# Optimization experiments

Measured on AMD Instinct MI355X. Metric: run time of the kernel, lower is better.

## Reference

```python
import jax, jax.numpy as jnp
import numpy as np

B, T, N, F_IN = 2, 4, 1024, 256
H, N_HIDDEN = 8, 128
SLOPE = 0.2
NEG_INF = -9e16


def setup_inputs() -> dict:
    key = jax.random.key(0)
    k1, k2, k3, k4 = jax.random.split(key, 4)
    h = jax.random.normal(k1, (B, T, N, F_IN), dtype=jnp.float32)
    adj_mat = jax.random.randint(k2, (N, N), 0, 2, dtype=jnp.int32)
    W = jax.random.normal(k3, (F_IN, H * N_HIDDEN), dtype=jnp.float32) * 0.05
    a = jax.random.normal(k4, (H, 2 * N_HIDDEN, 1), dtype=jnp.float32) * 0.05
    return {"h": h, "adj_mat": adj_mat, "W": W, "a": a}


def reference(h, adj_mat, W, a):
    b, t, n, _ = h.shape
    # linear transform: [B,T,N,F_in] @ [F_in, H*nh] -> [B,T,N,H*nh]
    ht = jnp.einsum('btjs,sh->btjh', h, W)
    # dropout is identity in eval mode
    ht = ht.reshape(b, t, n, H, N_HIDDEN).transpose(0, 1, 3, 2, 4)  # [B,T,H,N,nh]
    # additive attention scores
    a_src = a[:, :N_HIDDEN, :]   # [H, nh, 1]
    a_tgt = a[:, N_HIDDEN:, :]   # [H, nh, 1]
    src = jnp.einsum('bthnd,hdo->bthno', ht, a_src)  # [B,T,H,N,1]
    tgt = jnp.einsum('bthnd,hdo->bthno', ht, a_tgt)  # [B,T,H,N,1]
    e = src + jnp.swapaxes(tgt, -1, -2)              # [B,T,H,N,N]
    e = jnp.where(e >= 0, e, SLOPE * e)              # LeakyReLU
    e = jnp.where(adj_mat > 0, e, jnp.float32(NEG_INF))
    attention = jax.nn.softmax(e, axis=-1)
    # weighted aggregation: [B,T,H,N,N] @ [B,T,H,N,nh]
    h_prime = jnp.einsum('bthij,bthjd->bthid', attention, ht)
    # concat=False branch: mean over dim 0 (batch), as in the source
    return h_prime.mean(axis=0)  # [T,H,N,nh]
```

## Files before the change

### kernel.cpp

```cpp
#include <hip/hip_runtime.h>
#include <cstddef>
#include <cstdint>

#define B_ 2
#define T_ 4
#define N_ 1024
#define FIN_ 256
#define H_ 8
#define D_ 128
#define L2E_ 1.4426950408889634f

typedef __attribute__((ext_vector_type(8))) short short8;
typedef __attribute__((ext_vector_type(4))) float f32x4;

#define MFMA16(A, B, C) __builtin_amdgcn_mfma_f32_16x16x32_bf16((A), (B), (C), 0, 0, 0)

__device__ __forceinline__ unsigned short f2bf(float f) {
    uint32_t u = __float_as_uint(f);
    uint32_t r = (u + 0x7fffu + ((u >> 16) & 1u)) >> 16;
    return (unsigned short)r;
}

__device__ __forceinline__ uint32_t cvt_pk_bf16(float lo, float hi) {
    uint32_t r;
    asm volatile("v_cvt_pk_bf16_f32 %0, %1, %2" : "=v"(r) : "v"(lo), "v"(hi));
    return r;
}

__device__ __forceinline__ float fexp2(float x) {
#if __has_builtin(__builtin_amdgcn_exp2f)
    return __builtin_amdgcn_exp2f(x);
#else
    float r;
    asm("v_exp_f32 %0, %1" : "=v"(r) : "v"(x));
    return r;
#endif
}

__device__ __forceinline__ void load_lds16(const unsigned short* g, unsigned short* l) {
    __builtin_amdgcn_global_load_lds(
        (const __attribute__((address_space(1))) uint32_t*)g,
        (__attribute__((address_space(3))) uint32_t*)l, 16, 0, 0);
}

__global__ __launch_bounds__(256) void k_prep(const int* __restrict__ adj,
                                              const float* __restrict__ W,
                                              const float* __restrict__ a,
                                              unsigned short* __restrict__ Wt_bf,
                                              uint32_t* __restrict__ adjbits,
                                              float* __restrict__ wa) {
    __shared__ float wl[64][68];
    const int bid = blockIdx.x, tid = threadIdx.x;
    if (bid < 128) {
        const int w = bid * 256 + tid;
        const int i = w >> 5, jw = w & 31;
        const int4* p = (const int4*)(adj + (size_t)i * N_ + jw * 32);
        uint32_t bits = 0;
        #pragma unroll
        for (int q = 0; q < 8; ++q) {
            const int4 v = p[q];
            bits |= (uint32_t)(v.x > 0) << (q * 4 + 0);
            bits |= (uint32_t)(v.y > 0) << (q * 4 + 1);
            bits |= (uint32_t)(v.z > 0) << (q * 4 + 2);
            bits |= (uint32_t)(v.w > 0) << (q * 4 + 3);
        }
        adjbits[w] = bits;
    } else if (bid < 192) {
        const int tb  = bid - 128;
        const int hk0 = (tb >> 2) * 64;
        const int s0  = (tb & 3) * 64;
        {
            const int r  = tid >> 2;
            const int c0 = (tid & 3) * 16;
            #pragma unroll
            for (int k = 0; k < 4; ++k)
                *(float4*)&wl[r][c0 + k * 4] =
                    *(const float4*)(W + (size_t)(s0 + r) * (H_ * D_) + hk0 + c0 + k * 4);
        }
        __syncthreads();
        {
            const int r2 = tid >> 2;
            const int c2 = (tid & 3) * 16;
            unsigned short ob[16];
            #pragma unroll
            for (int k = 0; k < 16; ++k) ob[k] = f2bf(wl[c2 + k][r2]);
            unsigned short* dst = Wt_bf + (size_t)(hk0 + r2) * FIN_ + s0 + c2;
            *(uint4*)(dst)     = *(uint4*)&ob[0];
            *(uint4*)(dst + 8) = *(uint4*)&ob[8];
        }
    } else {
        const int o    = (bid - 192) * 256 + tid;
        const int head = o >> 9;
        const int st   = (o >> 8) & 1;
        const int s    = o & 255;
        const float* wr = W + (size_t)s * (H_ * D_) + head * D_;
        const float* ar = a + head * 256 + st * 128;
        float sum = 0.f;
        #pragma unroll
        for (int d = 0; d < 128; d += 4) {
            const float4 wv = *(const float4*)(wr + d);
            const float4 av = *(const float4*)(ar + d);
            sum += wv.x * av.x + wv.y * av.y + wv.z * av.z + wv.w * av.w;
        }
        wa[s * 16 + head * 2 + st] = sum;
    }
}

__global__ __launch_bounds__(256, 2) void k_gemm_sp(const float* __restrict__ h,
                                                    const unsigned short* __restrict__ Wt_bf,
                                                    const float* __restrict__ wa,
                                                    unsigned short* __restrict__ htT,
                                                    float* __restrict__ s1, float* __restrict__ s2,
                                                    float* __restrict__ t1, float* __restrict__ t2) {
    __shared__ __align__(16) char smem[24576];
    const int bid = blockIdx.x, tid = threadIdx.x;
    if (bid < 1024) {
        unsigned short* a_lds = (unsigned short*)smem;
        unsigned short* b_lds = (unsigned short*)(smem + 16384);
        const int xcd  = bid & 7;
        const int slot = bid >> 3;
        const int gid  = xcd * 8 + (slot >> 4);
        const int bt   = gid >> 3;
        const int n0   = (gid & 7) * 128;
        const int hk0  = (slot & 15) * 64;
        const int w = tid >> 6, lane = tid & 63;
        const int row16 = lane & 15, kgrp = lane >> 4;
        const int kswz = (kgrp ^ ((row16 >> 1) & 3)) * 8;
        const int ar  = tid >> 1;
        const int akh = tid & 1;
        const int asub = ar >> 4, arow = ar & 15;
        const int ax = (arow >> 1) & 3;
        const int aslot0 = ((akh * 2) ^ ax) * 8;
        const int aslot1 = ((akh * 2 + 1) ^ ax) * 8;
        const float* ga = h + ((size_t)bt * N_ + n0 + ar) * FIN_ + akh * 16;
        unsigned short* aw_ = a_lds + asub * 512 + arow * 32;
        const int brow = lane >> 2;
        const int bsb  = (lane & 3) ^ ((lane >> 3) & 3);
        const unsigned short* gb = Wt_bf + (size_t)(hk0 + w * 16 + brow) * FIN_ + bsb * 8;
        unsigned short* bw_ = b_lds + w * 512 + (size_t)lane * 8;

#define STAGE_AB(BUF, KS) {                                                    \
        const float* g = ga + (KS) * 32;                                       \
        const float4 f0 = *(const float4*)(g);                                 \
        const float4 f1 = *(const float4*)(g + 4);                             \
        const float4 f2 = *(const float4*)(g + 8);                             \
        const float4 f3 = *(const float4*)(g + 12);                            \
        uint4 o0, o1;                                                          \
        o0.x = cvt_pk_bf16(f0.x, f0.y); o0.y = cvt_pk_bf16(f0.z, f0.w);        \
        o0.z = cvt_pk_bf16(f1.x, f1.y); o0.w = cvt_pk_bf16(f1.z, f1.w);        \
        o1.x = cvt_pk_bf16(f2.x, f2.y); o1.y = cvt_pk_bf16(f2.z, f2.w);        \
        o1.z = cvt_pk_bf16(f3.x, f3.y); o1.w = cvt_pk_bf16(f3.z, f3.w);        \
        unsigned short* ad = aw_ + (BUF) * 4096;                               \
        *(uint4*)(ad + aslot0) = o0;                                           \
        *(uint4*)(ad + aslot1) = o1;                                           \
        load_lds16(gb + (KS) * 32, bw_ + (BUF) * 2048); }

        f32x4 acc[8];
        #pragma unroll
        for (int nt = 0; nt < 8; ++nt) acc[nt] = (f32x4){0.f, 0.f, 0.f, 0.f};

        STAGE_AB(0, 0)
        __syncthreads();
        for (int ks = 0; ks < 8; ++ks) {
            const int cur = ks & 1;
            if (ks < 7) STAGE_AB(cur ^ 1, ks + 1)
            const unsigned short* ab = a_lds + cur * 4096;
            const short8 bf = *(const short8*)(b_lds + cur * 2048 + w * 512 + row16 * 32 + kswz);
            #pragma unroll
            for (int nt = 0; nt < 8; ++nt) {
                const short8 af = *(const short8*)(ab + nt * 512 + row16 * 32 + kswz);
                acc[nt] = MFMA16(af, bf, acc[nt]);
            }
            __syncthreads();
        }
#undef STAGE_AB
        const int hk   = hk0 + w * 16 + row16;
        const int head = hk >> 7;
        const int d    = hk & 127;
        unsigned short* ob = htT + ((size_t)(bt * H_ + head) * D_ + d) * N_;
        #pragma unroll
        for (int nt = 0; nt < 8; ++nt) {
            ushort4 v;
            v.x = f2bf(acc[nt][0]); v.y = f2bf(acc[nt][1]);
            v.z = f2bf(acc[nt][2]); v.w = f2bf(acc[nt][3]);
            *(ushort4*)(ob + n0 + nt * 16 + kgrp * 4) = v;
        }
    } else {
        float (*was)[16] = (float(*)[16])smem;
        {
            const int f = tid * 16;
            #pragma unroll
            for (int k = 0; k < 4; ++k)
                *(float4*)&was[f >> 4][k * 4] = *(const float4*)(wa + f + k * 4);
        }
        __syncthreads();
        const int r = tid >> 2, q = tid & 3;
        const int R = (bid - 1024) * 64 + r;
        const float* hrow = h + (size_t)R * FIN_ + q * 64;
        float acc[16];
        #pragma unroll
        for (int o = 0; o < 16; ++o) acc[o] = 0.f;
        for (int k = 0; k < 64; k += 4) {
            const float4 hv = *(const float4*)(hrow + k);
            const int s = q * 64 + k;
            #pragma unroll
            for (int kk = 0; kk < 4; ++kk) {
                const float hs = (kk == 0) ? hv.x : (kk == 1) ? hv.y : (kk == 2) ? hv.z : hv.w;
                #pragma unroll
                for (int o = 0; o < 16; ++o) acc[o] += hs * was[s + kk][o];
            }
        }
        #pragma unroll
        for (int o = 0; o < 16; ++o) {
            acc[o] += __shfl_xor(acc[o], 1);
            acc[o] += __shfl_xor(acc[o], 2);
        }
        const int bt = R >> 10, n = R & 1023;
        #pragma unroll
        for (int k = 0; k < 4; ++k) {
            const int o = q * 4 + k;
            const int head = o >> 1;
            const size_t idx = ((size_t)(bt * H_ + head)) * N_ + n;
            const float v = acc[o];
            if (o & 1) { t1[idx] = v * L2E_; t2[idx] = v * (0.2f * L2E_); }
            else       { s1[idx] = v * L2E_; s2[idx] = v * (0.2f * L2E_); }
        }
    }
}

struct SC {
    float4 a1l, a1h, a2l, a2h;
    uint32_t mA, mB;
};

__global__ __launch_bounds__(256, 2) void k_attn(const unsigned short* __restrict__ htT,
                                                 const float* __restrict__ s1,
                                                 const float* __restrict__ s2,
                                                 const float* __restrict__ t1,
                                                 const float* __restrict__ t2,
                                                 const uint32_t* __restrict__ adjbits,
                                                 float* __restrict__ out) {
    __shared__ __align__(16) char smem[65536];
    unsigned short* stg = (unsigned short*)smem;
    const int xcd  = blockIdx.x & 7;
    const int slot = blockIdx.x >> 3;
    const int th   = xcd * 4 + (slot >> 4);
    const int i0   = (slot & 15) * 64;
    const int tid = threadIdx.x;
    const int w = tid >> 6, lane = tid & 63;
    const int b = w & 1, isub = w >> 1;
    const int row16 = lane & 15, kgrp = lane >> 4, jrel = kgrp * 8;
    const int kswz = (kgrp ^ ((row16 >> 1) & 3)) * 8;
    const int bth = b * (T_ * H_) + th;
    const int iA  = i0 + isub * 32 + row16;
    const int iB  = iA + 16;
    const float s1A = s1[(size_t)bth * N_ + iA], s2A = s2[(size_t)bth * N_ + iA];
    const float s1B = s1[(size_t)bth * N_ + iB], s2B = s2[(size_t)bth * N_ + iB];
    const float* t1b = t1 + (size_t)bth * N_;
    const float* t2b = t2 + (size_t)bth * N_;
    const uint32_t* adjA = adjbits + (size_t)iA * (N_ / 32);
    const uint32_t* adjB = adjbits + (size_t)iB * (N_ / 32);

    const int sb  = w >> 1;
    const int sd0 = (w & 1) * 64 + (lane >> 2);
    const int sj  = ((lane & 3) ^ ((lane >> 3) & 3)) * 8;
    const unsigned short* gstg = htT + ((size_t)(sb * (T_ * H_) + th) * D_ + sd0) * N_ + sj;
    unsigned short* lstg = stg + (size_t)w * 2048 + (size_t)lane * 8;

#define STAGE(BUF, T) {                                          \
        const unsigned short* gs = gstg + (size_t)(T) * 32;      \
        unsigned short* ls = lstg + (BUF) * 8192;                \
        load_lds16(gs,           ls);                            \
        load_lds16(gs + 16 * N_, ls + 512);                      \
        load_lds16(gs + 32 * N_, ls + 1024);                     \
        load_lds16(gs + 48 * N_, ls + 1536); }

#define LOADSC(S, T) {                                           \
        S.a1l = *(const float4*)(t1b + (T) * 32 + jrel);         \
        S.a1h = *(const float4*)(t1b + (T) * 32 + jrel + 4);     \
        S.a2l = *(const float4*)(t2b + (T) * 32 + jrel);         \
        S.a2h = *(const float4*)(t2b + (T) * 32 + jrel + 4);     \
        S.mA  = adjA[(T)];                                       \
        S.mB  = adjB[(T)]; }

    f32x4 accA[8], accB[8];
    #pragma unroll
    for (int nt = 0; nt < 8; ++nt) {
        accA[nt] = (f32x4){0.f, 0.f, 0.f, 0.f};
        accB[nt] = (f32x4){0.f, 0.f, 0.f, 0.f};
    }
    f32x4 daccA = (f32x4){0.f, 0.f, 0.f, 0.f};
    f32x4 daccB = (f32x4){0.f, 0.f, 0.f, 0.f};
    short8 ones8;
    {
        const short ov = (row16 == 0) ? (short)0x3F80 : (short)0;
        #pragma unroll
        for (int e = 0; e < 8; ++e) ones8[e] = ov;
    }
    const unsigned short* rdbase = stg + b * 4096 + row16 * 32 + kswz;

    SC scX, scY;

#define BODY(T, US, PS, TPF)                                                   \
    asm volatile("s_waitcnt vmcnt(14)" ::: "memory");                          \
    __builtin_amdgcn_s_barrier();                                              \
    asm volatile("" ::: "memory");                                             \
    STAGE(((T) + 3) & 3, ((T) + 3) & 31)                                       \
    LOADSC(PS, (TPF))                                                          \
    {                                                                          \
        const float tj1[8] = {US.a1l.x, US.a1l.y, US.a1l.z, US.a1l.w,          \
                              US.a1h.x, US.a1h.y, US.a1h.z, US.a1h.w};         \
        const float tj2[8] = {US.a2l.x, US.a2l.y, US.a2l.z, US.a2l.w,          \
                              US.a2h.x, US.a2h.y, US.a2h.z, US.a2h.w};         \
        const uint32_t mA = US.mA >> jrel;                                     \
        const uint32_t mB = US.mB >> jrel;                                     \
        float wvA[8], wvB[8];                                                  \
        _Pragma("unroll")                                                      \
        for (int e = 0; e < 8; ++e) {                                          \
            const float eA = fmaxf(s1A + tj1[e], s2A + tj2[e]);                \
            const float eB = fmaxf(s1B + tj1[e], s2B + tj2[e]);                \
            wvA[e] = ((mA >> e) & 1u) ? fexp2(eA) : 0.f;                       \
            wvB[e] = ((mB >> e) & 1u) ? fexp2(eB) : 0.f;                       \
        }                                                                      \
        short8 afA, afB;                                                       \
        _Pragma("unroll")                                                      \
        for (int p = 0; p < 4; ++p) {                                          \
            ((uint32_t*)&afA)[p] = cvt_pk_bf16(wvA[2 * p], wvA[2 * p + 1]);    \
            ((uint32_t*)&afB)[p] = cvt_pk_bf16(wvB[2 * p], wvB[2 * p + 1]);    \
        }                                                                      \
        const unsigned short* rb = rdbase + ((T) & 3) * 8192;                  \
        short8 bfr[8];                                                         \
        _Pragma("unroll")                                                      \
        for (int nt = 0; nt < 8; ++nt) bfr[nt] = *(const short8*)(rb + nt * 512); \
        _Pragma("unroll")                                                      \
        for (int nt = 0; nt < 8; ++nt) {                                       \
            accA[nt] = MFMA16(afA, bfr[nt], accA[nt]);                         \
            accB[nt] = MFMA16(afB, bfr[nt], accB[nt]);                         \
        }                                                                      \
        daccA = MFMA16(afA, ones8, daccA);                                     \
        daccB = MFMA16(afB, ones8, daccB);                                     \
    }

    STAGE(0, 0)
    STAGE(1, 1)
    STAGE(2, 2)
    LOADSC(scX, 0)

    for (int tt = 0; tt < 16; ++tt) {
        const int t0 = tt * 2;
        BODY(t0,     scX, scY, t0 + 1)
        BODY(t0 + 1, scY, scX, (t0 + 2) & 31)
    }
#undef BODY
#undef LOADSC
#undef STAGE

    __syncthreads();

    float ivA[4], ivB[4];
    #pragma unroll
    for (int r = 0; r < 4; ++r) {
        ivA[r] = __shfl(1.0f / daccA[r], kgrp * 16);
        ivB[r] = __shfl(1.0f / daccB[r], kgrp * 16);
    }

    float* comb = (float*)smem;
    if (b == 1) {
        #pragma unroll
        for (int nt = 0; nt < 8; ++nt)
            #pragma unroll
            for (int r = 0; r < 4; ++r) {
                const int il = isub * 32 + kgrp * 4 + r;
                const int d  = nt * 16 + row16;
                comb[il * 128 + d]        = accA[nt][r] * ivA[r];
                comb[(il + 16) * 128 + d] = accB[nt][r] * ivB[r];
            }
    }
    __syncthreads();
    if (b == 0) {
        #pragma unroll
        for (int nt = 0; nt < 8; ++nt)
            #pragma unroll
            for (int r = 0; r < 4; ++r) {
                const int il = isub * 32 + kgrp * 4 + r;
                const int d  = nt * 16 + row16;
                out[((size_t)th * N_ + i0 + il) * D_ + d] =
                    0.5f * (accA[nt][r] * ivA[r] + comb[il * 128 + d]);
                out[((size_t)th * N_ + i0 + il + 16) * D_ + d] =
                    0.5f * (accB[nt][r] * ivB[r] + comb[(il + 16) * 128 + d]);
            }
    }
}

extern "C" void kernel_launch(void* const* d_in, const int* in_sizes, int n_in,
                              void* d_out, int out_size, void* d_ws, size_t ws_size,
                              hipStream_t stream) {
    const float* h   = (const float*)d_in[0];
    const int*   adj = (const int*)d_in[1];
    const float* W   = (const float*)d_in[2];
    const float* a   = (const float*)d_in[3];
    float* out = (float*)d_out;

    char* p = (char*)d_ws;
    unsigned short* htT = (unsigned short*)p;  p += (size_t)B_ * T_ * H_ * D_ * N_ * 2;
    float* s1 = (float*)p;                     p += (size_t)B_ * T_ * H_ * N_ * 4;
    float* s2 = (float*)p;                     p += (size_t)B_ * T_ * H_ * N_ * 4;
    float* t1 = (float*)p;                     p += (size_t)B_ * T_ * H_ * N_ * 4;
    float* t2 = (float*)p;                     p += (size_t)B_ * T_ * H_ * N_ * 4;
    uint32_t* adjbits = (uint32_t*)p;          p += (size_t)N_ * N_ / 32 * 4;
    unsigned short* Wt_bf = (unsigned short*)p;p += (size_t)(H_ * D_) * FIN_ * 2;
    float* wa = (float*)p;

    k_prep<<<dim3(208), dim3(256), 0, stream>>>(adj, W, a, Wt_bf, adjbits, wa);
    k_gemm_sp<<<dim3(1152), dim3(256), 0, stream>>>(h, Wt_bf, wa, htT, s1, s2, t1, t2);
    k_attn<<<dim3(512), dim3(256), 0, stream>>>(htT, s1, s2, t1, t2, adjbits, out);
}
```

Before: 76.97 us.

## Restructure GEMM and attention pipelines to prefetch further and barrier less often

The projection GEMM now loads A from global into registers two k-steps ahead, writes it to LDS after the compute, and replaces __syncthreads with explicit waitcnt plus barrier. The attention loop now stages two j-tiles per barrier instead of one, which halves the barrier count and keeps score loads one tile ahead. The aim is to hide global latency and cut synchronisation overhead, at the cost of more live registers and fragile vmcnt accounting.

```diff
diff --git a/kernel.cpp b/kernel.cpp
--- a/kernel.cpp
+++ b/kernel.cpp
@@ -139,41 +139,55 @@
         const unsigned short* gb = Wt_bf + (size_t)(hk0 + w * 16 + brow) * FIN_ + bsb * 8;
         unsigned short* bw_ = b_lds + w * 512 + (size_t)lane * 8;
 
-#define STAGE_AB(BUF, KS) {                                                    \
+        float4 rf0, rf1, rf2, rf3;
+
+#define LOADA(KS) {                                                            \
         const float* g = ga + (KS) * 32;                                       \
-        const float4 f0 = *(const float4*)(g);                                 \
-        const float4 f1 = *(const float4*)(g + 4);                             \
-        const float4 f2 = *(const float4*)(g + 8);                             \
-        const float4 f3 = *(const float4*)(g + 12);                            \
+        rf0 = *(const float4*)(g);      rf1 = *(const float4*)(g + 4);         \
+        rf2 = *(const float4*)(g + 8);  rf3 = *(const float4*)(g + 12); }
+
+#define WRITEA(BUF) {                                                          \
         uint4 o0, o1;                                                          \
-        o0.x = cvt_pk_bf16(f0.x, f0.y); o0.y = cvt_pk_bf16(f0.z, f0.w);        \
-        o0.z = cvt_pk_bf16(f1.x, f1.y); o0.w = cvt_pk_bf16(f1.z, f1.w);        \
-        o1.x = cvt_pk_bf16(f2.x, f2.y); o1.y = cvt_pk_bf16(f2.z, f2.w);        \
-        o1.z = cvt_pk_bf16(f3.x, f3.y); o1.w = cvt_pk_bf16(f3.z, f3.w);        \
+        o0.x = cvt_pk_bf16(rf0.x, rf0.y); o0.y = cvt_pk_bf16(rf0.z, rf0.w);    \
+        o0.z = cvt_pk_bf16(rf1.x, rf1.y); o0.w = cvt_pk_bf16(rf1.z, rf1.w);    \
+        o1.x = cvt_pk_bf16(rf2.x, rf2.y); o1.y = cvt_pk_bf16(rf2.z, rf2.w);    \
+        o1.z = cvt_pk_bf16(rf3.x, rf3.y); o1.w = cvt_pk_bf16(rf3.z, rf3.w);    \
         unsigned short* ad = aw_ + (BUF) * 4096;                               \
         *(uint4*)(ad + aslot0) = o0;                                           \
-        *(uint4*)(ad + aslot1) = o1;                                           \
-        load_lds16(gb + (KS) * 32, bw_ + (BUF) * 2048); }
+        *(uint4*)(ad + aslot1) = o1; }
+
+#define COMPK(BUF) {                                                           \
+        const unsigned short* ab = a_lds + (BUF) * 4096;                       \
+        const short8 bfv = *(const short8*)(b_lds + (BUF) * 2048 + w * 512 + row16 * 32 + kswz); \
+        _Pragma("unroll")                                                      \
+        for (int nt = 0; nt < 8; ++nt) {                                       \
+            const short8 afv = *(const short8*)(ab + nt * 512 + row16 * 32 + kswz); \
+            acc[nt] = MFMA16(afv, bfv, acc[nt]);                               \
+        } }
 
         f32x4 acc[8];
         #pragma unroll
         for (int nt = 0; nt < 8; ++nt) acc[nt] = (f32x4){0.f, 0.f, 0.f, 0.f};
 
-        STAGE_AB(0, 0)
-        __syncthreads();
+        LOADA(0)
+        WRITEA(0)
+        load_lds16(gb, bw_);
+        LOADA(1)
+        asm volatile("s_waitcnt vmcnt(4) lgkmcnt(0)" ::: "memory");
+        __builtin_amdgcn_s_barrier();
+
         for (int ks = 0; ks < 8; ++ks) {
             const int cur = ks & 1;
-            if (ks < 7) STAGE_AB(cur ^ 1, ks + 1)
-            const unsigned short* ab = a_lds + cur * 4096;
-            const short8 bf = *(const short8*)(b_lds + cur * 2048 + w * 512 + row16 * 32 + kswz);
-            #pragma unroll
-            for (int nt = 0; nt < 8; ++nt) {
-                const short8 af = *(const short8*)(ab + nt * 512 + row16 * 32 + kswz);
-                acc[nt] = MFMA16(af, bf, acc[nt]);
-            }
-            __syncthreads();
-        }
-#undef STAGE_AB
+            WRITEA(cur ^ 1)
+            load_lds16(gb + ((ks + 1) & 7) * 32, bw_ + (cur ^ 1) * 2048);
+            LOADA((ks + 2) & 7)
+            COMPK(cur)
+            asm volatile("s_waitcnt vmcnt(4) lgkmcnt(0)" ::: "memory");
+            __builtin_amdgcn_s_barrier();
+        }
+#undef LOADA
+#undef WRITEA
+#undef COMPK
         const int hk   = hk0 + w * 16 + row16;
         const int head = hk >> 7;
         const int d    = hk & 127;
@@ -267,21 +281,21 @@
     const unsigned short* gstg = htT + ((size_t)(sb * (T_ * H_) + th) * D_ + sd0) * N_ + sj;
     unsigned short* lstg = stg + (size_t)w * 2048 + (size_t)lane * 8;
 
-#define STAGE(BUF, T) {                                          \
-        const unsigned short* gs = gstg + (size_t)(T) * 32;      \
+#define STAGE(BUF, T32) {                                        \
+        const unsigned short* gs = gstg + (size_t)(T32) * 32;    \
         unsigned short* ls = lstg + (BUF) * 8192;                \
         load_lds16(gs,           ls);                            \
         load_lds16(gs + 16 * N_, ls + 512);                      \
         load_lds16(gs + 32 * N_, ls + 1024);                     \
         load_lds16(gs + 48 * N_, ls + 1536); }
 
-#define LOADSC(S, T) {                                           \
-        S.a1l = *(const float4*)(t1b + (T) * 32 + jrel);         \
-        S.a1h = *(const float4*)(t1b + (T) * 32 + jrel + 4);     \
-        S.a2l = *(const float4*)(t2b + (T) * 32 + jrel);         \
-        S.a2h = *(const float4*)(t2b + (T) * 32 + jrel + 4);     \
-        S.mA  = adjA[(T)];                                       \
-        S.mB  = adjB[(T)]; }
+#define LOADSC(S, T32) {                                         \
+        S.a1l = *(const float4*)(t1b + (T32) * 32 + jrel);       \
+        S.a1h = *(const float4*)(t1b + (T32) * 32 + jrel + 4);   \
+        S.a2l = *(const float4*)(t2b + (T32) * 32 + jrel);       \
+        S.a2h = *(const float4*)(t2b + (T32) * 32 + jrel + 4);   \
+        S.mA  = adjA[(T32)];                                     \
+        S.mB  = adjB[(T32)]; }
 
     f32x4 accA[8], accB[8];
     #pragma unroll
@@ -299,21 +313,16 @@
     }
     const unsigned short* rdbase = stg + b * 4096 + row16 * 32 + kswz;
 
-    SC scX, scY;
-
-#define BODY(T, US, PS, TPF)                                                   \
-    asm volatile("s_waitcnt vmcnt(14)" ::: "memory");                          \
-    __builtin_amdgcn_s_barrier();                                              \
-    asm volatile("" ::: "memory");                                             \
-    STAGE(((T) + 3) & 3, ((T) + 3) & 31)                                       \
-    LOADSC(PS, (TPF))                                                          \
+    SC scA, scB;
+
+#define SUBP(BUFIDX, SCS, TNEXT)                                               \
     {                                                                          \
-        const float tj1[8] = {US.a1l.x, US.a1l.y, US.a1l.z, US.a1l.w,          \
-                              US.a1h.x, US.a1h.y, US.a1h.z, US.a1h.w};         \
-        const float tj2[8] = {US.a2l.x, US.a2l.y, US.a2l.z, US.a2l.w,          \
-                              US.a2h.x, US.a2h.y, US.a2h.z, US.a2h.w};         \
-        const uint32_t mA = US.mA >> jrel;                                     \
-        const uint32_t mB = US.mB >> jrel;                                     \
+        const float tj1[8] = {SCS.a1l.x, SCS.a1l.y, SCS.a1l.z, SCS.a1l.w,      \
+                              SCS.a1h.x, SCS.a1h.y, SCS.a1h.z, SCS.a1h.w};     \
+        const float tj2[8] = {SCS.a2l.x, SCS.a2l.y, SCS.a2l.z, SCS.a2l.w,      \
+                              SCS.a2h.x, SCS.a2h.y, SCS.a2h.z, SCS.a2h.w};     \
+        const uint32_t mA = SCS.mA >> jrel;                                    \
+        const uint32_t mB = SCS.mB >> jrel;                                    \
         float wvA[8], wvB[8];                                                  \
         _Pragma("unroll")                                                      \
         for (int e = 0; e < 8; ++e) {                                          \
@@ -328,7 +337,8 @@
             ((uint32_t*)&afA)[p] = cvt_pk_bf16(wvA[2 * p], wvA[2 * p + 1]);    \
             ((uint32_t*)&afB)[p] = cvt_pk_bf16(wvB[2 * p], wvB[2 * p + 1]);    \
         }                                                                      \
-        const unsigned short* rb = rdbase + ((T) & 3) * 8192;                  \
+        LOADSC(SCS, (TNEXT))                                                   \
+        const unsigned short* rb = rdbase + (BUFIDX) * 8192;                   \
         short8 bfr[8];                                                         \
         _Pragma("unroll")                                                      \
         for (int nt = 0; nt < 8; ++nt) bfr[nt] = *(const short8*)(rb + nt * 512); \
@@ -343,15 +353,21 @@
 
     STAGE(0, 0)
     STAGE(1, 1)
-    STAGE(2, 2)
-    LOADSC(scX, 0)
-
-    for (int tt = 0; tt < 16; ++tt) {
-        const int t0 = tt * 2;
-        BODY(t0,     scX, scY, t0 + 1)
-        BODY(t0 + 1, scY, scX, (t0 + 2) & 31)
-    }
-#undef BODY
+    LOADSC(scA, 0)
+    LOADSC(scB, 1)
+
+    for (int T = 0; T < 16; ++T) {
+        const int pair  = T & 1;
+        const int npair = pair ^ 1;
+        asm volatile("s_waitcnt vmcnt(12)" ::: "memory");
+        __builtin_amdgcn_s_barrier();
+        asm volatile("" ::: "memory");
+        STAGE(npair * 2,     (2 * T + 2) & 31)
+        STAGE(npair * 2 + 1, (2 * T + 3) & 31)
+        SUBP(pair * 2,     scA, (2 * T + 2) & 31)
+        SUBP(pair * 2 + 1, scB, (2 * T + 3) & 31)
+    }
+#undef SUBP
 #undef LOADSC
 #undef STAGE
 
```

Result: no change. 77.13 us (+0.2%).
